# Kernel tuning notes

Hardware: AMD Instinct MI355X
Metric: run time of the kernel (lower is better)

The kernel has to match this reference:

```python
import jax, jax.numpy as jnp
import numpy as np

N_NODES = 50000
N_EDGES = 600000
D_IN = 128
HID = 128
N_SAGE = 2          # num_layers - 1
N_GRAPHS = 512
BN_EPS = 1e-5


def setup_inputs() -> dict:
    key = jax.random.key(0)
    ks = jax.random.split(key, 12)
    s = 1.0 / np.sqrt(HID)
    x = jax.random.normal(ks[0], (N_NODES, D_IN), dtype=jnp.float32)
    edge_index = jax.random.randint(ks[1], (2, N_EDGES), 0, N_NODES, dtype=jnp.int32)
    batch = jnp.sort(jax.random.randint(ks[2], (N_NODES,), 0, N_GRAPHS, dtype=jnp.int32))
    # GIN MLP: Linear(D_IN,HID) -> ReLU -> Linear(HID,HID)
    gin_w1 = jax.random.normal(ks[3], (D_IN, HID), dtype=jnp.float32) * s
    gin_b1 = jnp.zeros((HID,), jnp.float32)
    gin_w2 = jax.random.normal(ks[4], (HID, HID), dtype=jnp.float32) * s
    gin_b2 = jnp.zeros((HID,), jnp.float32)
    # SAGEConv layers: lin_l (neighbors, with bias), lin_r (root, no bias)
    sage_wl = jax.random.normal(ks[5], (N_SAGE, HID, HID), dtype=jnp.float32) * s
    sage_bl = jnp.zeros((N_SAGE, HID), jnp.float32)
    sage_wr = jax.random.normal(ks[6], (N_SAGE, HID, HID), dtype=jnp.float32) * s
    # BatchNorm per layer (3 layers)
    bn_gamma = jnp.ones((1 + N_SAGE, HID), jnp.float32)
    bn_beta = jnp.zeros((1 + N_SAGE, HID), jnp.float32)
    return {"x": x, "edge_index": edge_index, "batch": batch,
            "gin_w1": gin_w1, "gin_b1": gin_b1, "gin_w2": gin_w2, "gin_b2": gin_b2,
            "sage_wl": sage_wl, "sage_bl": sage_bl, "sage_wr": sage_wr,
            "bn_gamma": bn_gamma, "bn_beta": bn_beta}


def _batchnorm(h, gamma, beta):
    # training-mode BN over the node dimension (biased variance, as torch)
    mu = jnp.mean(h, axis=0)
    var = jnp.var(h, axis=0)
    return gamma * (h - mu) * jax.lax.rsqrt(var + BN_EPS) + beta


def reference(x, edge_index, batch, gin_w1, gin_b1, gin_w2, gin_b2,
              sage_wl, sage_bl, sage_wr, bn_gamma, bn_beta):
    n = x.shape[0]
    src, dst = edge_index[0], edge_index[1]

    # ---- Layer 0: GINConv (eps=0): mlp(x + sum_{j->i} x_j) ----
    agg = jax.ops.segment_sum(x[src], dst, num_segments=n)  # [N, D_IN]
    h = x + agg
    h = jax.nn.relu(h @ gin_w1 + gin_b1) @ gin_w2 + gin_b2
    h = jax.nn.relu(_batchnorm(h, bn_gamma[0], bn_beta[0]))
    # dropout is identity (eval mode)

    # degree for mean aggregation (shared across SAGE layers)
    deg = jax.ops.segment_sum(jnp.ones((src.shape[0],), h.dtype), dst, num_segments=n)
    inv_deg = (1.0 / jnp.maximum(deg, 1.0))[:, None]  # [N,1]

    # ---- SAGE layers: lin_l(mean_{j->i} h_j) + lin_r(h_i) ----
    for l in range(N_SAGE):
        neigh = jax.ops.segment_sum(h[src], dst, num_segments=n) * inv_deg
        h = neigh @ sage_wl[l] + sage_bl[l] + h @ sage_wr[l]
        h = jax.nn.relu(_batchnorm(h, bn_gamma[l + 1], bn_beta[l + 1]))

    # ---- global mean pool over batch ids ----
    sums = jax.ops.segment_sum(h, batch, num_segments=N_GRAPHS)  # [G, HID]
    counts = jax.ops.segment_sum(jnp.ones((n,), h.dtype), batch, num_segments=N_GRAPHS)
    return sums / jnp.maximum(counts, 1.0)[:, None]
```

## Files before the change

kernel.cpp:

```cpp
#include <hip/hip_runtime.h>

#define N_NODES 50000
#define N_EDGES 600000
#define HID 128
#define N_GRAPHS 512
#define BN_EPS 1e-5f
#define INV_N (1.0f / 50000.0f)
#define SLICE_STRIDE 1600000
#define NSLICES 4
#define GATHER_GROUPS 782
#define IDXCAP 1536

typedef __attribute__((ext_vector_type(8))) short bf16x8;
typedef __attribute__((ext_vector_type(4))) float f32x4;

__device__ __forceinline__ unsigned short f2b(float f) {
    unsigned u = __float_as_uint(f);
    return (unsigned short)((u + 0x7FFFu + ((u >> 16) & 1u)) >> 16);
}
__device__ __forceinline__ float b2f(unsigned short h) {
    return __uint_as_float(((unsigned)h) << 16);
}

__device__ __forceinline__ float stats_sum(const float* __restrict__ s, int idx) {
    float v = 0.f;
#pragma unroll
    for (int r = 0; r < 8; r++) v += s[r * 256 + idx];
    return v;
}

#define CONVX_BLOCKS 6250
#define WCONV_BLOCKS 384
#define DEG_BLOCKS   2344
__global__ __launch_bounds__(256) void prep_kernel(
    const float* __restrict__ x, const float* __restrict__ gw1, const float* __restrict__ gw2,
    const float* __restrict__ swl, const float* __restrict__ swr, const int* __restrict__ dst,
    unsigned short* __restrict__ x16, unsigned short* __restrict__ wt, int* __restrict__ deg)
{
    int b = blockIdx.x;
    int t = threadIdx.x;
    if (b < CONVX_BLOCKS) {
        int gid = b * 256 + t;
        int i = gid >> 5, l = gid & 31;
        if (i >= N_NODES) return;
        int c0 = l * 4;
        float4 v = *(const float4*)(x + (size_t)i * 128 + c0);
        ushort4 o;
        o.x = f2b(v.x); o.y = f2b(v.y); o.z = f2b(v.z); o.w = f2b(v.w);
        *(ushort4*)(x16 + (size_t)(l >> 3) * SLICE_STRIDE + (size_t)i * 32 + (l & 7) * 4) = o;
    } else if (b < CONVX_BLOCKS + WCONV_BLOCKS) {
        int gid = (b - CONVX_BLOCKS) * 256 + t;
        int m = gid >> 14;
        int e = gid & 16383;
        int k = e >> 7;
        int n = e & 127;
        const float* src = (m == 0) ? gw1 : (m == 1) ? gw2 : (m == 2) ? swl
                         : (m == 3) ? swr : (m == 4) ? (swl + 16384) : (swr + 16384);
        wt[m * 16384 + n * 128 + k] = f2b(src[k * 128 + n]);
    } else {
        int e = (b - CONVX_BLOCKS - WCONV_BLOCKS) * 256 + t;
        if (e < N_EDGES) atomicAdd(&deg[dst[e]], 1);
    }
}

#define ALLOC_BLOCKS 196
__global__ __launch_bounds__(256) void alloc_kernel(int* __restrict__ cursor,
                                                    int* __restrict__ row_beg,
                                                    float* __restrict__ inv_deg,
                                                    int* __restrict__ total,
                                                    const int* __restrict__ batch,
                                                    int* __restrict__ gstart) {
    if (blockIdx.x >= ALLOC_BLOCKS) {
        int g = (blockIdx.x - ALLOC_BLOCKS) * 256 + threadIdx.x;
        if (g > N_GRAPHS) return;
        int lo = 0, hi = N_NODES;
        while (lo < hi) {
            int mid = (lo + hi) >> 1;
            if (batch[mid] < g) lo = mid + 1; else hi = mid;
        }
        gstart[g] = lo;
        return;
    }
    __shared__ int tmp[256];
    __shared__ int base;
    int i = blockIdx.x * 256 + threadIdx.x;
    int d = (i < N_NODES) ? cursor[i] : 0;
    tmp[threadIdx.x] = d;
    __syncthreads();
#pragma unroll
    for (int off = 1; off < 256; off <<= 1) {
        int v = (threadIdx.x >= off) ? tmp[threadIdx.x - off] : 0;
        __syncthreads();
        tmp[threadIdx.x] += v;
        __syncthreads();
    }
    if (threadIdx.x == 255) base = atomicAdd(total, tmp[255]);
    __syncthreads();
    if (i < N_NODES) {
        int b = base + tmp[threadIdx.x] - d;
        row_beg[i] = b;
        cursor[i] = b;
        inv_deg[i] = 1.0f / fmaxf((float)d, 1.0f);
    }
}

__global__ void csr_fill_kernel(const int* __restrict__ src, const int* __restrict__ dst,
                                int* __restrict__ cursor, unsigned short* __restrict__ csr_src, int nE) {
    int e = blockIdx.x * blockDim.x + threadIdx.x;
    if (e < nE) {
        int pos = atomicAdd(&cursor[dst[e]], 1);
        csr_src[pos] = (unsigned short)src[e];
    }
}

template<bool AFF>
__global__ __launch_bounds__(256, 6) void gather_slice_kernel(
    const unsigned short* __restrict__ feat_s,
    const int* __restrict__ row_beg, const int* __restrict__ row_end,
    const unsigned short* __restrict__ csr_src,
    const float* __restrict__ inv_deg,
    const float* __restrict__ stats_in, const float* __restrict__ gamma,
    const float* __restrict__ beta,
    unsigned short* __restrict__ agg_s, unsigned short* __restrict__ hact_s)
{
    __shared__ unsigned short idxbuf[IDXCAP];
    __shared__ float csc[32], css[32];
    const int t = threadIdx.x;
    const int slice = blockIdx.x & 3;
    const int grp = blockIdx.x >> 2;
    const int node0 = grp * 64;
    const int nlast = (node0 + 63 < N_NODES) ? node0 + 63 : N_NODES - 1;
    const int node = node0 + (t >> 2);
    const int l8 = (t & 3) * 8;
    const unsigned short* fbase = feat_s + (size_t)slice * SLICE_STRIDE + l8;

    if (AFF && t < 32) {
        int col = slice * 32 + t;
        float mu = stats_sum(stats_in, col) * INV_N;
        float var = stats_sum(stats_in, 128 + col) * INV_N - mu * mu;
        float rs = rsqrtf(var + BN_EPS);
        float c = gamma[col] * rs;
        csc[t] = c;
        css[t] = beta[col] - mu * c;
    }

    const int ebeg = row_beg[node0];
    const int ecnt = row_end[nlast] - ebeg;
    const bool lds_ok = (ecnt <= IDXCAP);
    if (lds_ok)
        for (int i = t; i < ecnt; i += 256) idxbuf[i] = csr_src[ebeg + i];
    __syncthreads();
    if (node >= N_NODES) return;

    float cc[8], ss[8];
    if (AFF) {
#pragma unroll
        for (int j = 0; j < 8; j++) { cc[j] = csc[l8 + j]; ss[j] = css[l8 + j]; }
    }

    const int beg = row_beg[node];
    const int deg = row_end[node] - beg;

    float a[8];
#pragma unroll
    for (int j = 0; j < 8; j++) a[j] = 0.f;

    if (lds_ok) {
        const int off = beg - ebeg;
        int e = 0;
        for (; e + 7 < deg; e += 8) {
            int s[8];
#pragma unroll
            for (int u = 0; u < 8; u++) s[u] = idxbuf[off + e + u];
            bf16x8 v[8];
#pragma unroll
            for (int u = 0; u < 8; u++)
                v[u] = *(const bf16x8*)(fbase + (size_t)s[u] * 32);
#pragma unroll
            for (int u = 0; u < 8; u++)
#pragma unroll
                for (int j = 0; j < 8; j++) {
                    float tv = b2f((unsigned short)v[u][j]);
                    if (AFF) tv = fmaxf(tv * cc[j] + ss[j], 0.f);
                    a[j] += tv;
                }
        }
        for (; e + 3 < deg; e += 4) {
            int s[4];
#pragma unroll
            for (int u = 0; u < 4; u++) s[u] = idxbuf[off + e + u];
            bf16x8 v[4];
#pragma unroll
            for (int u = 0; u < 4; u++)
                v[u] = *(const bf16x8*)(fbase + (size_t)s[u] * 32);
#pragma unroll
            for (int u = 0; u < 4; u++)
#pragma unroll
                for (int j = 0; j < 8; j++) {
                    float tv = b2f((unsigned short)v[u][j]);
                    if (AFF) tv = fmaxf(tv * cc[j] + ss[j], 0.f);
                    a[j] += tv;
                }
        }
        for (; e < deg; e++) {
            int s0 = idxbuf[off + e];
            bf16x8 v0 = *(const bf16x8*)(fbase + (size_t)s0 * 32);
#pragma unroll
            for (int j = 0; j < 8; j++) {
                float tv = b2f((unsigned short)v0[j]);
                if (AFF) tv = fmaxf(tv * cc[j] + ss[j], 0.f);
                a[j] += tv;
            }
        }
    } else {
        for (int e = beg; e < beg + deg; e++) {
            int s0 = csr_src[e];
            bf16x8 v0 = *(const bf16x8*)(fbase + (size_t)s0 * 32);
#pragma unroll
            for (int j = 0; j < 8; j++) {
                float tv = b2f((unsigned short)v0[j]);
                if (AFF) tv = fmaxf(tv * cc[j] + ss[j], 0.f);
                a[j] += tv;
            }
        }
    }

    if (AFF) {
        float sc = inv_deg[node];
#pragma unroll
        for (int j = 0; j < 8; j++) a[j] *= sc;
    }
    bf16x8 o;
#pragma unroll
    for (int j = 0; j < 8; j++) o[j] = (short)f2b(a[j]);
    *(bf16x8*)(agg_s + (size_t)slice * SLICE_STRIDE + (size_t)node * 32 + l8) = o;

    if (AFF) {
        bf16x8 v = *(const bf16x8*)(fbase + (size_t)node * 32);
        bf16x8 h;
#pragma unroll
        for (int j = 0; j < 8; j++)
            h[j] = (short)f2b(fmaxf(b2f((unsigned short)v[j]) * cc[j] + ss[j], 0.f));
        *(bf16x8*)(hact_s + (size_t)slice * SLICE_STRIDE + (size_t)node * 32 + l8) = h;
    }
}

__global__ __launch_bounds__(256, 2) void gemm_gin_kernel(
    const unsigned short* __restrict__ X, const unsigned short* __restrict__ AGG,
    const unsigned short* __restrict__ W1t, const unsigned short* __restrict__ W2t,
    const float* __restrict__ b1, const float* __restrict__ b2,
    float* __restrict__ stats, unsigned short* __restrict__ Cb,
    int M, int ntiles)
{
    __shared__ unsigned short t1[32][136];
    __shared__ float red[2][128];

    const int t = threadIdx.x;
    const int wave = t >> 6;
    const int lane = t & 63;
    const int colhalf = wave & 1;
    const int rowpair = wave >> 1;
    const int m16 = lane & 15;
    const int quad = lane >> 4;
    const int k0 = quad * 8;
    const int colbase = colhalf * 64;
    const int lrow = rowpair * 16 + m16;

    const bf16x8 zero8 = {0, 0, 0, 0, 0, 0, 0, 0};

    bf16x8 w1f[4][4], w2f[4][4];
#pragma unroll
    for (int ct = 0; ct < 4; ct++) {
        int col = colbase + ct * 16 + m16;
#pragma unroll
        for (int kc = 0; kc < 4; kc++) {
            w1f[ct][kc] = *(const bf16x8*)(W1t + (size_t)col * 128 + kc * 32 + k0);
            w2f[ct][kc] = *(const bf16x8*)(W2t + (size_t)col * 128 + kc * 32 + k0);
        }
    }
    f32x4 bs1[4], bs2[4];
#pragma unroll
    for (int ct = 0; ct < 4; ct++) {
        bs1[ct] = *(const f32x4*)(b1 + colbase + ct * 16 + quad * 4);
        bs2[ct] = *(const f32x4*)(b2 + colbase + ct * 16 + quad * 4);
    }

    float psum[4][4], psq[4][4];
#pragma unroll
    for (int ct = 0; ct < 4; ct++)
#pragma unroll
        for (int r = 0; r < 4; r++) { psum[ct][r] = 0.f; psq[ct][r] = 0.f; }

    for (int tile = blockIdx.x; tile < ntiles; tile += gridDim.x) {
        int arow = tile * 32 + rowpair * 16 + m16;
        bool aok = arow < M;

        bf16x8 a[4];
#pragma unroll
        for (int kc = 0; kc < 4; kc++) {
            if (aok) {
                size_t aoff = (size_t)kc * SLICE_STRIDE + (size_t)arow * 32 + quad * 8;
                bf16x8 vx = *(const bf16x8*)(X + aoff);
                bf16x8 vg = *(const bf16x8*)(AGG + aoff);
                bf16x8 r;
#pragma unroll
                for (int i = 0; i < 8; i++)
                    r[i] = (short)f2b(b2f((unsigned short)vx[i]) + b2f((unsigned short)vg[i]));
                a[kc] = r;
            } else {
                a[kc] = zero8;
            }
        }

        f32x4 acc[4];
#pragma unroll
        for (int ct = 0; ct < 4; ct++) acc[ct] = (f32x4){0.f, 0.f, 0.f, 0.f};
#pragma unroll
        for (int kc = 0; kc < 4; kc++)
#pragma unroll
            for (int ct = 0; ct < 4; ct++)
                acc[ct] = __builtin_amdgcn_mfma_f32_16x16x32_bf16(w1f[ct][kc], a[kc], acc[ct], 0, 0, 0);

        __syncthreads();
#pragma unroll
        for (int ct = 0; ct < 4; ct++) {
            f32x4 v = acc[ct] + bs1[ct];
            ushort4 o;
            o.x = f2b(fmaxf(v[0], 0.f));
            o.y = f2b(fmaxf(v[1], 0.f));
            o.z = f2b(fmaxf(v[2], 0.f));
            o.w = f2b(fmaxf(v[3], 0.f));
            *(ushort4*)&t1[lrow][colbase + ct * 16 + quad * 4] = o;
        }
        __syncthreads();

        bf16x8 ta[4];
#pragma unroll
        for (int kc = 0; kc < 4; kc++)
            ta[kc] = *(const bf16x8*)&t1[lrow][kc * 32 + k0];

        f32x4 acc2[4];
#pragma unroll
        for (int ct = 0; ct < 4; ct++) acc2[ct] = (f32x4){0.f, 0.f, 0.f, 0.f};
#pragma unroll
        for (int kc = 0; kc < 4; kc++)
#pragma unroll
            for (int ct = 0; ct < 4; ct++)
                acc2[ct] = __builtin_amdgcn_mfma_f32_16x16x32_bf16(w2f[ct][kc], ta[kc], acc2[ct], 0, 0, 0);

        if (arow < M) {
#pragma unroll
            for (int ct = 0; ct < 4; ct++) {
                f32x4 v = acc2[ct] + bs2[ct];
#pragma unroll
                for (int r = 0; r < 4; r++) { psum[ct][r] += v[r]; psq[ct][r] += v[r] * v[r]; }
                ushort4 o;
                o.x = f2b(v[0]); o.y = f2b(v[1]); o.z = f2b(v[2]); o.w = f2b(v[3]);
                int cloc = ct * 16 + quad * 4;
                int cs = colhalf * 2 + (cloc >> 5);
                int coff = cloc & 31;
                *(ushort4*)(Cb + (size_t)cs * SLICE_STRIDE + (size_t)arow * 32 + coff) = o;
            }
        }
    }

#pragma unroll
    for (int ct = 0; ct < 4; ct++)
#pragma unroll
        for (int r = 0; r < 4; r++) {
#pragma unroll
            for (int mask = 1; mask <= 8; mask <<= 1) {
                psum[ct][r] += __shfl_xor(psum[ct][r], mask, 64);
                psq[ct][r]  += __shfl_xor(psq[ct][r], mask, 64);
            }
        }
    __syncthreads();
    if (m16 == 0) {
#pragma unroll
        for (int ct = 0; ct < 4; ct++)
#pragma unroll
            for (int r = 0; r < 4; r++)
                red[rowpair][colbase + ct * 16 + quad * 4 + r] = psum[ct][r];
    }
    __syncthreads();
    if (t < 128) atomicAdd(&stats[(blockIdx.x & 7) * 256 + t], red[0][t] + red[1][t]);
    __syncthreads();
    if (m16 == 0) {
#pragma unroll
        for (int ct = 0; ct < 4; ct++)
#pragma unroll
            for (int r = 0; r < 4; r++)
                red[rowpair][colbase + ct * 16 + quad * 4 + r] = psq[ct][r];
    }
    __syncthreads();
    if (t < 128) atomicAdd(&stats[(blockIdx.x & 7) * 256 + 128 + t], red[0][t] + red[1][t]);
}

__global__ __launch_bounds__(256) void gemm_dual_kernel(
    const unsigned short* __restrict__ A1, const unsigned short* __restrict__ A2,
    const unsigned short* __restrict__ W1t, const unsigned short* __restrict__ W2t,
    const float* __restrict__ bias, float* __restrict__ stats,
    unsigned short* __restrict__ Cb, int M, int ntiles)
{
    __shared__ float red[128];

    const int t = threadIdx.x;
    const int wave = t >> 6;
    const int lane = t & 63;
    const int m16 = lane & 15;
    const int quad = lane >> 4;
    const int k0 = quad * 8;
    const int colbase = wave * 32;

    const bf16x8 zero8 = {0, 0, 0, 0, 0, 0, 0, 0};

    bf16x8 w1f[2][4], w2f[2][4];
#pragma unroll
    for (int ct = 0; ct < 2; ct++) {
        int col = colbase + ct * 16 + m16;
#pragma unroll
        for (int kc = 0; kc < 4; kc++) {
            w1f[ct][kc] = *(const bf16x8*)(W1t + (size_t)col * 128 + kc * 32 + k0);
            w2f[ct][kc] = *(const bf16x8*)(W2t + (size_t)col * 128 + kc * 32 + k0);
        }
    }
    f32x4 bs[2];
#pragma unroll
    for (int ct = 0; ct < 2; ct++)
        bs[ct] = *(const f32x4*)(bias + colbase + ct * 16 + quad * 4);

    float psum[2][4], psq[2][4];
#pragma unroll
    for (int ct = 0; ct < 2; ct++)
#pragma unroll
        for (int r = 0; r < 4; r++) { psum[ct][r] = 0.f; psq[ct][r] = 0.f; }

    bf16x8 a1[4], a2[4], a1n[4], a2n[4];

    int tile = blockIdx.x;
    if (tile < ntiles) {
        int arow = tile * 16 + m16;
        bool aok = arow < M;
#pragma unroll
        for (int kc = 0; kc < 4; kc++) {
            size_t aoff = (size_t)kc * SLICE_STRIDE + (size_t)arow * 32 + quad * 8;
            a1[kc] = aok ? *(const bf16x8*)(A1 + aoff) : zero8;
            a2[kc] = aok ? *(const bf16x8*)(A2 + aoff) : zero8;
        }
    }

    for (; tile < ntiles; tile += gridDim.x) {
        int nt = tile + gridDim.x;
        if (nt < ntiles) {
            int arow = nt * 16 + m16;
            bool aok = arow < M;
#pragma unroll
            for (int kc = 0; kc < 4; kc++) {
                size_t aoff = (size_t)kc * SLICE_STRIDE + (size_t)arow * 32 + quad * 8;
                a1n[kc] = aok ? *(const bf16x8*)(A1 + aoff) : zero8;
                a2n[kc] = aok ? *(const bf16x8*)(A2 + aoff) : zero8;
            }
        }

        f32x4 acc[2];
        acc[0] = (f32x4){0.f, 0.f, 0.f, 0.f};
        acc[1] = (f32x4){0.f, 0.f, 0.f, 0.f};
#pragma unroll
        for (int kc = 0; kc < 4; kc++) {
#pragma unroll
            for (int ct = 0; ct < 2; ct++) {
                acc[ct] = __builtin_amdgcn_mfma_f32_16x16x32_bf16(w1f[ct][kc], a1[kc], acc[ct], 0, 0, 0);
                acc[ct] = __builtin_amdgcn_mfma_f32_16x16x32_bf16(w2f[ct][kc], a2[kc], acc[ct], 0, 0, 0);
            }
        }

        int orow = tile * 16 + m16;
        if (orow < M) {
#pragma unroll
            for (int ct = 0; ct < 2; ct++) {
                f32x4 v = acc[ct] + bs[ct];
#pragma unroll
                for (int r = 0; r < 4; r++) { psum[ct][r] += v[r]; psq[ct][r] += v[r] * v[r]; }
                ushort4 o;
                o.x = f2b(v[0]); o.y = f2b(v[1]); o.z = f2b(v[2]); o.w = f2b(v[3]);
                *(ushort4*)(Cb + (size_t)wave * SLICE_STRIDE + (size_t)orow * 32 + ct * 16 + quad * 4) = o;
            }
        }

        if (nt < ntiles) {
            a1[0] = a1n[0]; a1[1] = a1n[1]; a1[2] = a1n[2]; a1[3] = a1n[3];
            a2[0] = a2n[0]; a2[1] = a2n[1]; a2[2] = a2n[2]; a2[3] = a2n[3];
        }
    }

#pragma unroll
    for (int ct = 0; ct < 2; ct++)
#pragma unroll
        for (int r = 0; r < 4; r++) {
#pragma unroll
            for (int mask = 1; mask <= 8; mask <<= 1) {
                psum[ct][r] += __shfl_xor(psum[ct][r], mask, 64);
                psq[ct][r]  += __shfl_xor(psq[ct][r], mask, 64);
            }
        }
    if (m16 == 0) {
#pragma unroll
        for (int ct = 0; ct < 2; ct++)
#pragma unroll
            for (int r = 0; r < 4; r++)
                red[colbase + ct * 16 + quad * 4 + r] = psum[ct][r];
    }
    __syncthreads();
    if (t < 128) atomicAdd(&stats[(blockIdx.x & 7) * 256 + t], red[t]);
    __syncthreads();
    if (m16 == 0) {
#pragma unroll
        for (int ct = 0; ct < 2; ct++)
#pragma unroll
            for (int r = 0; r < 4; r++)
                red[colbase + ct * 16 + quad * 4 + r] = psq[ct][r];
    }
    __syncthreads();
    if (t < 128) atomicAdd(&stats[(blockIdx.x & 7) * 256 + 128 + t], red[t]);
}

__global__ __launch_bounds__(256) void pool_mean_kernel(const unsigned short* __restrict__ h_s,
                                                        const int* __restrict__ gstart,
                                                        const float* __restrict__ stats,
                                                        const float* __restrict__ gamma,
                                                        const float* __restrict__ beta,
                                                        float* __restrict__ out) {
    __shared__ float red[16][128];
    int g = blockIdx.x;
    int t = threadIdx.x;
    int grp = t >> 4;
    int ci = t & 15;
    int c0 = ci * 8;
    float c[8], b[8];
#pragma unroll
    for (int j = 0; j < 8; j++) {
        int col = c0 + j;
        float mu = stats_sum(stats, col) * INV_N;
        float var = stats_sum(stats, 128 + col) * INV_N - mu * mu;
        float rs = rsqrtf(var + BN_EPS);
        c[j] = gamma[col] * rs;
        b[j] = beta[col] - mu * c[j];
    }
    int beg = gstart[g];
    int end = gstart[g + 1];
    float sa[8];
#pragma unroll
    for (int j = 0; j < 8; j++) sa[j] = 0.f;
    const unsigned short* base = h_s + (size_t)(ci >> 2) * SLICE_STRIDE + (ci & 3) * 8;
    for (int i = beg + grp; i < end; i += 16) {
        bf16x8 v = *(const bf16x8*)(base + (size_t)i * 32);
#pragma unroll
        for (int j = 0; j < 8; j++)
            sa[j] += fmaxf(b2f((unsigned short)v[j]) * c[j] + b[j], 0.f);
    }
#pragma unroll
    for (int j = 0; j < 8; j++) red[grp][c0 + j] = sa[j];
    __syncthreads();
    if (t < 128) {
        float cnt = fmaxf((float)(end - beg), 1.0f);
        float tot = 0.f;
#pragma unroll
        for (int r = 0; r < 16; r++) tot += red[r][t];
        out[(size_t)g * 128 + t] = tot / cnt;
    }
}

extern "C" void kernel_launch(void* const* d_in, const int* in_sizes, int n_in,
                              void* d_out, int out_size, void* d_ws, size_t ws_size,
                              hipStream_t stream) {
    const float* x    = (const float*)d_in[0];
    const int*   ei   = (const int*)d_in[1];
    const int*   src  = ei;
    const int*   dst  = ei + N_EDGES;
    const int*   batch = (const int*)d_in[2];
    const float* gw1  = (const float*)d_in[3];
    const float* gb1  = (const float*)d_in[4];
    const float* gw2  = (const float*)d_in[5];
    const float* gb2  = (const float*)d_in[6];
    const float* swl  = (const float*)d_in[7];
    const float* sbl  = (const float*)d_in[8];
    const float* swr  = (const float*)d_in[9];
    const float* bng  = (const float*)d_in[10];
    const float* bnb  = (const float*)d_in[11];
    float* out = (float*)d_out;

    float* ws = (float*)d_ws;
    unsigned short* x16_s  = (unsigned short*)(ws + 0);
    unsigned short* agg_s  = (unsigned short*)(ws + 3200000);
    unsigned short* hact_s = (unsigned short*)(ws + 6400000);
    unsigned short* hpre_s = (unsigned short*)(ws + 9600000);
    unsigned short* wt     = (unsigned short*)(ws + 12800000);
    float*          inv_deg= ws + 12850000;
    int*            row_beg= (int*)(ws + 12900000);
    int*            cursor = (int*)(ws + 12950000);
    int*            total  = cursor + 50000;
    float*          stats  = (float*)(cursor + 50001);
    unsigned short* csr_src= (unsigned short*)(ws + 13100000);
    int*            gstart = (int*)(ws + 13700000);

    const int ggrid = 512;
    const int ntiles32 = (N_NODES + 31) / 32;
    const int ntiles16 = (N_NODES + 15) / 16;
    const int gather_grid = GATHER_GROUPS * NSLICES;

    hipMemsetAsync(cursor, 0, (50001 + 3 * 8 * 256) * sizeof(int), stream);

    prep_kernel<<<CONVX_BLOCKS + WCONV_BLOCKS + DEG_BLOCKS, 256, 0, stream>>>(
        x, gw1, gw2, swl, swr, dst, x16_s, wt, cursor);

    alloc_kernel<<<ALLOC_BLOCKS + 3, 256, 0, stream>>>(cursor, row_beg, inv_deg, total, batch, gstart);
    csr_fill_kernel<<<(N_EDGES + 255) / 256, 256, 0, stream>>>(src, dst, cursor, csr_src, N_EDGES);

    gather_slice_kernel<false><<<gather_grid, 256, 0, stream>>>(
        x16_s, row_beg, cursor, csr_src, nullptr, nullptr, nullptr, nullptr, agg_s, nullptr);
    gemm_gin_kernel<<<ggrid, 256, 0, stream>>>(
        x16_s, agg_s, wt + 0 * 16384, wt + 1 * 16384, gb1, gb2,
        stats + 0 * 2048, hpre_s, N_NODES, ntiles32);

    gather_slice_kernel<true><<<gather_grid, 256, 0, stream>>>(
        hpre_s, row_beg, cursor, csr_src, inv_deg,
        stats + 0 * 2048, bng + 0 * HID, bnb + 0 * HID, agg_s, hact_s);
    gemm_dual_kernel<<<ggrid, 256, 0, stream>>>(
        agg_s, hact_s, wt + 2 * 16384, wt + 3 * 16384, sbl + 0 * HID,
        stats + 1 * 2048, hpre_s, N_NODES, ntiles16);

    gather_slice_kernel<true><<<gather_grid, 256, 0, stream>>>(
        hpre_s, row_beg, cursor, csr_src, inv_deg,
        stats + 1 * 2048, bng + 1 * HID, bnb + 1 * HID, agg_s, hact_s);
    gemm_dual_kernel<<<ggrid, 256, 0, stream>>>(
        agg_s, hact_s, wt + 4 * 16384, wt + 5 * 16384, sbl + 1 * HID,
        stats + 2 * 2048, hpre_s, N_NODES, ntiles16);

    pool_mean_kernel<<<N_GRAPHS, 256, 0, stream>>>(
        hpre_s, gstart, stats + 2 * 2048, bng + 2 * HID, bnb + 2 * HID, out);
}
```

Measured before the change: 347.5 us.

## Use 16-column feature slices and fuse BN-ReLU of root features into dual GEMM

Feature storage changes from four 32-column slices to eight 16-column slices, so each gathered row fetch is 32 bytes and the gather grid covers 128 nodes per block with two lanes per node. The gather kernel no longer writes a separate activated root-feature buffer. Instead the dual GEMM recomputes BN scale and shift from the stats and applies affine plus ReLU to the pre-activation tile in registers before the MFMA. This removes one full N×128 bf16 write and read per SAGE layer and shrinks the slice each gather block touches. In exchange the GEMM does extra conversion arithmetic, and gather loads are narrower.

```diff
diff --git a/kernel.cpp b/kernel.cpp
--- a/kernel.cpp
+++ b/kernel.cpp
@@ -6,10 +6,10 @@
 #define N_GRAPHS 512
 #define BN_EPS 1e-5f
 #define INV_N (1.0f / 50000.0f)
-#define SLICE_STRIDE 1600000
-#define NSLICES 4
-#define GATHER_GROUPS 782
-#define IDXCAP 1536
+#define SLICE_STRIDE 800000
+#define NSLICES 8
+#define GATHER_GROUPS 391
+#define IDXCAP 4096
 
 typedef __attribute__((ext_vector_type(8))) short bf16x8;
 typedef __attribute__((ext_vector_type(4))) float f32x4;
@@ -47,7 +47,7 @@
         float4 v = *(const float4*)(x + (size_t)i * 128 + c0);
         ushort4 o;
         o.x = f2b(v.x); o.y = f2b(v.y); o.z = f2b(v.z); o.w = f2b(v.w);
-        *(ushort4*)(x16 + (size_t)(l >> 3) * SLICE_STRIDE + (size_t)i * 32 + (l & 7) * 4) = o;
+        *(ushort4*)(x16 + (size_t)(l >> 2) * SLICE_STRIDE + (size_t)i * 16 + (l & 3) * 4) = o;
     } else if (b < CONVX_BLOCKS + WCONV_BLOCKS) {
         int gid = (b - CONVX_BLOCKS) * 256 + t;
         int m = gid >> 14;
@@ -121,21 +121,21 @@
     const float* __restrict__ inv_deg,
     const float* __restrict__ stats_in, const float* __restrict__ gamma,
     const float* __restrict__ beta,
-    unsigned short* __restrict__ agg_s, unsigned short* __restrict__ hact_s)
+    unsigned short* __restrict__ agg_s)
 {
     __shared__ unsigned short idxbuf[IDXCAP];
-    __shared__ float csc[32], css[32];
+    __shared__ float csc[16], css[16];
     const int t = threadIdx.x;
-    const int slice = blockIdx.x & 3;
-    const int grp = blockIdx.x >> 2;
-    const int node0 = grp * 64;
-    const int nlast = (node0 + 63 < N_NODES) ? node0 + 63 : N_NODES - 1;
-    const int node = node0 + (t >> 2);
-    const int l8 = (t & 3) * 8;
+    const int slice = blockIdx.x & 7;
+    const int grp = blockIdx.x >> 3;
+    const int node0 = grp * 128;
+    const int nlast = (node0 + 127 < N_NODES) ? node0 + 127 : N_NODES - 1;
+    const int node = node0 + (t >> 1);
+    const int l8 = (t & 1) * 8;
     const unsigned short* fbase = feat_s + (size_t)slice * SLICE_STRIDE + l8;
 
-    if (AFF && t < 32) {
-        int col = slice * 32 + t;
+    if (AFF && t < 16) {
+        int col = slice * 16 + t;
         float mu = stats_sum(stats_in, col) * INV_N;
         float var = stats_sum(stats_in, 128 + col) * INV_N - mu * mu;
         float rs = rsqrtf(var + BN_EPS);
@@ -175,7 +175,7 @@
             bf16x8 v[8];
 #pragma unroll
             for (int u = 0; u < 8; u++)
-                v[u] = *(const bf16x8*)(fbase + (size_t)s[u] * 32);
+                v[u] = *(const bf16x8*)(fbase + (size_t)s[u] * 16);
 #pragma unroll
             for (int u = 0; u < 8; u++)
 #pragma unroll
@@ -192,7 +192,7 @@
             bf16x8 v[4];
 #pragma unroll
             for (int u = 0; u < 4; u++)
-                v[u] = *(const bf16x8*)(fbase + (size_t)s[u] * 32);
+                v[u] = *(const bf16x8*)(fbase + (size_t)s[u] * 16);
 #pragma unroll
             for (int u = 0; u < 4; u++)
 #pragma unroll
@@ -204,7 +204,7 @@
         }
         for (; e < deg; e++) {
             int s0 = idxbuf[off + e];
-            bf16x8 v0 = *(const bf16x8*)(fbase + (size_t)s0 * 32);
+            bf16x8 v0 = *(const bf16x8*)(fbase + (size_t)s0 * 16);
 #pragma unroll
             for (int j = 0; j < 8; j++) {
                 float tv = b2f((unsigned short)v0[j]);
@@ -215,7 +215,7 @@
     } else {
         for (int e = beg; e < beg + deg; e++) {
             int s0 = csr_src[e];
-            bf16x8 v0 = *(const bf16x8*)(fbase + (size_t)s0 * 32);
+            bf16x8 v0 = *(const bf16x8*)(fbase + (size_t)s0 * 16);
 #pragma unroll
             for (int j = 0; j < 8; j++) {
                 float tv = b2f((unsigned short)v0[j]);
@@ -233,16 +233,7 @@
     bf16x8 o;
 #pragma unroll
     for (int j = 0; j < 8; j++) o[j] = (short)f2b(a[j]);
-    *(bf16x8*)(agg_s + (size_t)slice * SLICE_STRIDE + (size_t)node * 32 + l8) = o;
-
-    if (AFF) {
-        bf16x8 v = *(const bf16x8*)(fbase + (size_t)node * 32);
-        bf16x8 h;
-#pragma unroll
-        for (int j = 0; j < 8; j++)
-            h[j] = (short)f2b(fmaxf(b2f((unsigned short)v[j]) * cc[j] + ss[j], 0.f));
-        *(bf16x8*)(hact_s + (size_t)slice * SLICE_STRIDE + (size_t)node * 32 + l8) = h;
-    }
+    *(bf16x8*)(agg_s + (size_t)slice * SLICE_STRIDE + (size_t)node * 16 + l8) = o;
 }
 
 __global__ __launch_bounds__(256, 2) void gemm_gin_kernel(
@@ -299,7 +290,8 @@
 #pragma unroll
         for (int kc = 0; kc < 4; kc++) {
             if (aok) {
-                size_t aoff = (size_t)kc * SLICE_STRIDE + (size_t)arow * 32 + quad * 8;
+                size_t aoff = (size_t)(kc * 2 + (quad >> 1)) * SLICE_STRIDE
+                            + (size_t)arow * 16 + (quad & 1) * 8;
                 bf16x8 vx = *(const bf16x8*)(X + aoff);
                 bf16x8 vg = *(const bf16x8*)(AGG + aoff);
                 bf16x8 r;
@@ -356,10 +348,8 @@
                 for (int r = 0; r < 4; r++) { psum[ct][r] += v[r]; psq[ct][r] += v[r] * v[r]; }
                 ushort4 o;
                 o.x = f2b(v[0]); o.y = f2b(v[1]); o.z = f2b(v[2]); o.w = f2b(v[3]);
-                int cloc = ct * 16 + quad * 4;
-                int cs = colhalf * 2 + (cloc >> 5);
-                int coff = cloc & 31;
-                *(ushort4*)(Cb + (size_t)cs * SLICE_STRIDE + (size_t)arow * 32 + coff) = o;
+                int cs = (colbase >> 4) + ct;
+                *(ushort4*)(Cb + (size_t)cs * SLICE_STRIDE + (size_t)arow * 16 + quad * 4) = o;
             }
         }
     }
@@ -397,12 +387,16 @@
 }
 
 __global__ __launch_bounds__(256) void gemm_dual_kernel(
-    const unsigned short* __restrict__ A1, const unsigned short* __restrict__ A2,
+    const unsigned short* __restrict__ A1, const unsigned short* __restrict__ Hp,
     const unsigned short* __restrict__ W1t, const unsigned short* __restrict__ W2t,
-    const float* __restrict__ bias, float* __restrict__ stats,
+    const float* __restrict__ bias,
+    const float* __restrict__ stats_in, const float* __restrict__ gamma,
+    const float* __restrict__ beta,
+    float* __restrict__ stats_out,
     unsigned short* __restrict__ Cb, int M, int ntiles)
 {
     __shared__ float red[128];
+    __shared__ float csc[128], css[128];
 
     const int t = threadIdx.x;
     const int wave = t >> 6;
@@ -414,6 +408,26 @@
 
     const bf16x8 zero8 = {0, 0, 0, 0, 0, 0, 0, 0};
 
+    if (t < 128) {
+        float mu = stats_sum(stats_in, t) * INV_N;
+        float var = stats_sum(stats_in, 128 + t) * INV_N - mu * mu;
+        float rs = rsqrtf(var + BN_EPS);
+        float c = gamma[t] * rs;
+        csc[t] = c;
+        css[t] = beta[t] - mu * c;
+    }
+    __syncthreads();
+
+    f32x4 acA[4], acB[4], asA[4], asB[4];
+#pragma unroll
+    for (int kc = 0; kc < 4; kc++) {
+        int col0 = kc * 32 + quad * 8;
+        acA[kc] = *(const f32x4*)&csc[col0];
+        acB[kc] = *(const f32x4*)&csc[col0 + 4];
+        asA[kc] = *(const f32x4*)&css[col0];
+        asB[kc] = *(const f32x4*)&css[col0 + 4];
+    }
+
     bf16x8 w1f[2][4], w2f[2][4];
 #pragma unroll
     for (int ct = 0; ct < 2; ct++) {
@@ -443,9 +457,10 @@
         bool aok = arow < M;
 #pragma unroll
         for (int kc = 0; kc < 4; kc++) {
-            size_t aoff = (size_t)kc * SLICE_STRIDE + (size_t)arow * 32 + quad * 8;
+            size_t aoff = (size_t)(kc * 2 + (quad >> 1)) * SLICE_STRIDE
+                        + (size_t)arow * 16 + (quad & 1) * 8;
             a1[kc] = aok ? *(const bf16x8*)(A1 + aoff) : zero8;
-            a2[kc] = aok ? *(const bf16x8*)(A2 + aoff) : zero8;
+            a2[kc] = aok ? *(const bf16x8*)(Hp + aoff) : zero8;
         }
     }
 
@@ -456,9 +471,10 @@
             bool aok = arow < M;
 #pragma unroll
             for (int kc = 0; kc < 4; kc++) {
-                size_t aoff = (size_t)kc * SLICE_STRIDE + (size_t)arow * 32 + quad * 8;
+                size_t aoff = (size_t)(kc * 2 + (quad >> 1)) * SLICE_STRIDE
+                            + (size_t)arow * 16 + (quad & 1) * 8;
                 a1n[kc] = aok ? *(const bf16x8*)(A1 + aoff) : zero8;
-                a2n[kc] = aok ? *(const bf16x8*)(A2 + aoff) : zero8;
+                a2n[kc] = aok ? *(const bf16x8*)(Hp + aoff) : zero8;
             }
         }
 
@@ -467,10 +483,17 @@
         acc[1] = (f32x4){0.f, 0.f, 0.f, 0.f};
 #pragma unroll
         for (int kc = 0; kc < 4; kc++) {
+            bf16x8 a2c;
+#pragma unroll
+            for (int j = 0; j < 4; j++)
+                a2c[j] = (short)f2b(fmaxf(b2f((unsigned short)a2[kc][j]) * acA[kc][j] + asA[kc][j], 0.f));
+#pragma unroll
+            for (int j = 0; j < 4; j++)
+                a2c[4 + j] = (short)f2b(fmaxf(b2f((unsigned short)a2[kc][4 + j]) * acB[kc][j] + asB[kc][j], 0.f));
 #pragma unroll
             for (int ct = 0; ct < 2; ct++) {
                 acc[ct] = __builtin_amdgcn_mfma_f32_16x16x32_bf16(w1f[ct][kc], a1[kc], acc[ct], 0, 0, 0);
-                acc[ct] = __builtin_amdgcn_mfma_f32_16x16x32_bf16(w2f[ct][kc], a2[kc], acc[ct], 0, 0, 0);
+                acc[ct] = __builtin_amdgcn_mfma_f32_16x16x32_bf16(w2f[ct][kc], a2c, acc[ct], 0, 0, 0);
             }
         }
 
@@ -483,7 +506,8 @@
                 for (int r = 0; r < 4; r++) { psum[ct][r] += v[r]; psq[ct][r] += v[r] * v[r]; }
                 ushort4 o;
                 o.x = f2b(v[0]); o.y = f2b(v[1]); o.z = f2b(v[2]); o.w = f2b(v[3]);
-                *(ushort4*)(Cb + (size_t)wave * SLICE_STRIDE + (size_t)orow * 32 + ct * 16 + quad * 4) = o;
+                int cs = wave * 2 + ct;
+                *(ushort4*)(Cb + (size_t)cs * SLICE_STRIDE + (size_t)orow * 16 + quad * 4) = o;
             }
         }
 
@@ -511,7 +535,7 @@
                 red[colbase + ct * 16 + quad * 4 + r] = psum[ct][r];
     }
     __syncthreads();
-    if (t < 128) atomicAdd(&stats[(blockIdx.x & 7) * 256 + t], red[t]);
+    if (t < 128) atomicAdd(&stats_out[(blockIdx.x & 7) * 256 + t], red[t]);
     __syncthreads();
     if (m16 == 0) {
 #pragma unroll
@@ -521,7 +545,7 @@
                 red[colbase + ct * 16 + quad * 4 + r] = psq[ct][r];
     }
     __syncthreads();
-    if (t < 128) atomicAdd(&stats[(blockIdx.x & 7) * 256 + 128 + t], red[t]);
+    if (t < 128) atomicAdd(&stats_out[(blockIdx.x & 7) * 256 + 128 + t], red[t]);
 }
 
 __global__ __launch_bounds__(256) void pool_mean_kernel(const unsigned short* __restrict__ h_s,
@@ -551,9 +575,9 @@
     float sa[8];
 #pragma unroll
     for (int j = 0; j < 8; j++) sa[j] = 0.f;
-    const unsigned short* base = h_s + (size_t)(ci >> 2) * SLICE_STRIDE + (ci & 3) * 8;
+    const unsigned short* base = h_s + (size_t)(ci >> 1) * SLICE_STRIDE + (ci & 1) * 8;
     for (int i = beg + grp; i < end; i += 16) {
-        bf16x8 v = *(const bf16x8*)(base + (size_t)i * 32);
+        bf16x8 v = *(const bf16x8*)(base + (size_t)i * 16);
 #pragma unroll
         for (int j = 0; j < 8; j++)
             sa[j] += fmaxf(b2f((unsigned short)v[j]) * c[j] + b[j], 0.f);
@@ -592,8 +616,8 @@
     float* ws = (float*)d_ws;
     unsigned short* x16_s  = (unsigned short*)(ws + 0);
     unsigned short* agg_s  = (unsigned short*)(ws + 3200000);
-    unsigned short* hact_s = (unsigned short*)(ws + 6400000);
-    unsigned short* hpre_s = (unsigned short*)(ws + 9600000);
+    unsigned short* h_a    = (unsigned short*)(ws + 6400000);
+    unsigned short* h_b    = (unsigned short*)(ws + 9600000);
     unsigned short* wt     = (unsigned short*)(ws + 12800000);
     float*          inv_deg= ws + 12850000;
     int*            row_beg= (int*)(ws + 12900000);
@@ -617,25 +641,27 @@
     csr_fill_kernel<<<(N_EDGES + 255) / 256, 256, 0, stream>>>(src, dst, cursor, csr_src, N_EDGES);
 
     gather_slice_kernel<false><<<gather_grid, 256, 0, stream>>>(
-        x16_s, row_beg, cursor, csr_src, nullptr, nullptr, nullptr, nullptr, agg_s, nullptr);
+        x16_s, row_beg, cursor, csr_src, nullptr, nullptr, nullptr, nullptr, agg_s);
     gemm_gin_kernel<<<ggrid, 256, 0, stream>>>(
         x16_s, agg_s, wt + 0 * 16384, wt + 1 * 16384, gb1, gb2,
-        stats + 0 * 2048, hpre_s, N_NODES, ntiles32);
+        stats + 0 * 2048, h_a, N_NODES, ntiles32);
 
     gather_slice_kernel<true><<<gather_grid, 256, 0, stream>>>(
-        hpre_s, row_beg, cursor, csr_src, inv_deg,
-        stats + 0 * 2048, bng + 0 * HID, bnb + 0 * HID, agg_s, hact_s);
+        h_a, row_beg, cursor, csr_src, inv_deg,
+        stats + 0 * 2048, bng + 0 * HID, bnb + 0 * HID, agg_s);
     gemm_dual_kernel<<<ggrid, 256, 0, stream>>>(
-        agg_s, hact_s, wt + 2 * 16384, wt + 3 * 16384, sbl + 0 * HID,
-        stats + 1 * 2048, hpre_s, N_NODES, ntiles16);
+        agg_s, h_a, wt + 2 * 16384, wt + 3 * 16384, sbl + 0 * HID,
+        stats + 0 * 2048, bng + 0 * HID, bnb + 0 * HID,
+        stats + 1 * 2048, h_b, N_NODES, ntiles16);
 
     gather_slice_kernel<true><<<gather_grid, 256, 0, stream>>>(
-        hpre_s, row_beg, cursor, csr_src, inv_deg,
-        stats + 1 * 2048, bng + 1 * HID, bnb + 1 * HID, agg_s, hact_s);
+        h_b, row_beg, cursor, csr_src, inv_deg,
+        stats + 1 * 2048, bng + 1 * HID, bnb + 1 * HID, agg_s);
     gemm_dual_kernel<<<ggrid, 256, 0, stream>>>(
-        agg_s, hact_s, wt + 4 * 16384, wt + 5 * 16384, sbl + 1 * HID,
-        stats + 2 * 2048, hpre_s, N_NODES, ntiles16);
+        agg_s, h_b, wt + 4 * 16384, wt + 5 * 16384, sbl + 1 * HID,
+        stats + 1 * 2048, bng + 1 * HID, bnb + 1 * HID,
+        stats + 2 * 2048, h_a, N_NODES, ntiles16);
 
     pool_mean_kernel<<<N_GRAPHS, 256, 0, stream>>>(
-        hpre_s, gstart, stats + 2 * 2048, bng + 2 * HID, bnb + 2 * HID, out);
-}
+        h_a, gstart, stats + 2 * 2048, bng + 2 * HID, bnb + 2 * HID, out);
+}
```

Measured after the change: 352.4 us. Within noise of the previous version (+1.4%).
